# Performance work log

Measured on AMD Instinct MI355X. Metric: run time of the kernel, lower is better.

## Reference

```python
import jax, jax.numpy as jnp
import numpy as np

DEPTH = 100
HIDDEN = 1024
SHIFT = 25  # number of zeros prepended by the Shift module
LINEARITY = 0.97


def setup_inputs() -> dict:
    key = jax.random.key(0)
    ks = jax.random.split(key, 9)
    IN, OUT, B = 512, 512, 4096
    x = jax.random.normal(ks[0], (B, IN), dtype=jnp.float32)
    # torch Linear weight shape: [out, in]; xavier/kaiming init approximated by scaled normals
    fc1_w = jax.random.normal(ks[1], (HIDDEN, IN), dtype=jnp.float32) * (1.0 / np.sqrt(IN))
    fc1_b = jnp.zeros((HIDDEN,), dtype=jnp.float32)
    W1 = jax.random.normal(ks[2], (DEPTH, HIDDEN, HIDDEN), dtype=jnp.float32) * (1.0 / np.sqrt(HIDDEN))
    b1 = jnp.zeros((DEPTH, HIDDEN), dtype=jnp.float32)
    W2 = jax.random.normal(ks[3], (DEPTH, HIDDEN, HIDDEN), dtype=jnp.float32) * (np.sqrt(2.0) / np.sqrt(HIDDEN))
    b2 = jnp.zeros((DEPTH, HIDDEN), dtype=jnp.float32)
    fc2_w = jax.random.normal(ks[4], (OUT, HIDDEN), dtype=jnp.float32) * (1.0 / np.sqrt(HIDDEN))
    fc2_b = jnp.zeros((OUT,), dtype=jnp.float32)
    return {"x": x, "fc1_w": fc1_w, "fc1_b": fc1_b, "W1": W1, "b1": b1,
            "W2": W2, "b2": b2, "fc2_w": fc2_w, "fc2_b": fc2_b}


def _shift(x):
    # Shift: cat 25 zeros in front along last dim, then slice back to original width
    z = jnp.zeros_like(x[..., :SHIFT])
    return jnp.concatenate([z, x[..., :-SHIFT]], axis=-1)


def reference(x, fc1_w, fc1_b, W1, b1, W2, b2, fc2_w, fc2_b):
    x = x @ fc1_w.T + fc1_b  # [B, HIDDEN]

    def block(h, params):
        w1, bb1, w2, bb2 = params
        r = _shift(h)                       # shifted input is the residual
        a = jnp.maximum(r @ w1.T + bb1, 0)  # fc1 + clamp(min=0)
        y = a @ w2.T + bb2                  # fc2
        out = LINEARITY * r + (1.0 - LINEARITY) * y
        return out, None

    x, _ = jax.lax.scan(block, x, (W1, b1, W2, b2))
    return x @ fc2_w.T + fc2_b
```

## Files before the change

### kernel.cpp

```cpp
#include <hip/hip_runtime.h>
#include <cstdint>
#include <cstddef>

#define DEPTH 100
#define HID 1024
#define MROWS 4096

typedef _Float16 half8 __attribute__((ext_vector_type(8)));
typedef float floatx4 __attribute__((ext_vector_type(4)));

__device__ __forceinline__ void gload_lds16(const void* g, void* l) {
    __builtin_amdgcn_global_load_lds((const __attribute__((address_space(1))) void*)g,
                                     (__attribute__((address_space(3))) void*)l,
                                     16, 0, 0);
}

template<int MODE>
__global__ __launch_bounds__(512, 1)
void gemm_f(const _Float16* __restrict__ A, const _Float16* __restrict__ B,
            const float* __restrict__ bias, const float* __restrict__ hold,
            float* __restrict__ hnew, _Float16* __restrict__ rnext,
            _Float16* __restrict__ aout, float* __restrict__ outp,
            int N, int K, int rshift, int nbnl)
{
    __shared__ _Float16 As[3][128 * 64];
    __shared__ _Float16 Bs[3][128 * 64];

    const int tid = threadIdx.x;
    const int l   = tid & 63;
    const int w   = tid >> 6;
    const int wm  = w >> 2;
    const int wn  = w & 3;

    const int cpx = gridDim.x >> 3;
    const int b0  = blockIdx.x;
    const int bid = (b0 & 7) * cpx + (b0 >> 3);
    const int bn  = bid & ((1 << nbnl) - 1);
    const int bm  = bid >> nbnl;

    floatx4 acc[4][2];
    const floatx4 zero = {0.f, 0.f, 0.f, 0.f};
    #pragma unroll
    for (int i = 0; i < 4; ++i)
        #pragma unroll
        for (int j = 0; j < 2; ++j) acc[i][j] = zero;

    const int lr = l >> 3;
    const int lj = l & 7;
    const int sw = (l & 7) << 4;

    auto stage = [&](int buf, int kt) {
        #pragma unroll
        for (int q = 0; q < 2; ++q) {
            const int c   = w * 2 + q;
            const int row = c * 8 + lr;
            const int jch = lj ^ (row & 7);
            gload_lds16((const void*)(A + (size_t)(bm * 128 + row) * K + kt * 64 + jch * 8),
                        (void*)((char*)As[buf] + c * 1024));
        }
        #pragma unroll
        for (int q = 0; q < 2; ++q) {
            const int c   = w * 2 + q;
            const int row = c * 8 + lr;
            const int jch = lj ^ (row & 7);
            gload_lds16((const void*)(B + (size_t)(bn * 128 + row) * K + kt * 64 + jch * 8),
                        (void*)((char*)Bs[buf] + c * 1024));
        }
    };

    auto compute = [&](int buf) {
        #pragma unroll
        for (int kk = 0; kk < 2; ++kk) {
            half8 af[4], bf[2];
            #pragma unroll
            for (int fi = 0; fi < 4; ++fi) {
                const int off = ((wm * 64 + fi * 16 + (l & 15)) * 128 + kk * 64 + ((l >> 4) << 4)) ^ sw;
                af[fi] = *(const half8*)((const char*)As[buf] + off);
            }
            #pragma unroll
            for (int fj = 0; fj < 2; ++fj) {
                const int off = ((wn * 32 + fj * 16 + (l & 15)) * 128 + kk * 64 + ((l >> 4) << 4)) ^ sw;
                bf[fj] = *(const half8*)((const char*)Bs[buf] + off);
            }
            __builtin_amdgcn_s_setprio(1);
            #pragma unroll
            for (int fi = 0; fi < 4; ++fi)
                #pragma unroll
                for (int fj = 0; fj < 2; ++fj)
                    acc[fi][fj] = __builtin_amdgcn_mfma_f32_16x16x32_f16(af[fi], bf[fj], acc[fi][fj], 0, 0, 0);
            __builtin_amdgcn_s_setprio(0);
        }
    };

    const int nkt = K >> 6;
    stage(0, 0);
    if (nkt > 1) stage(1, 1);
    int cur = 0;
    for (int kt = 0; kt < nkt; ++kt) {
        if (kt + 2 < nkt) {
            int n2 = cur + 2; if (n2 >= 3) n2 -= 3;
            stage(n2, kt + 2);
        }
        const int rem   = nkt - 1 - kt;
        const int ahead = rem < 2 ? rem : 2;
        if (ahead == 2)      asm volatile("s_waitcnt vmcnt(8)" ::: "memory");
        else if (ahead == 1) asm volatile("s_waitcnt vmcnt(4)" ::: "memory");
        else                 asm volatile("s_waitcnt vmcnt(0)" ::: "memory");
        __builtin_amdgcn_s_barrier();
        __builtin_amdgcn_sched_barrier(0);
        compute(cur);
        __builtin_amdgcn_s_barrier();
        cur = (cur + 1 == 3) ? 0 : cur + 1;
    }

    const float C1 = 0.97f;
    const float C2 = (float)(1.0 - 0.97);
    const int colb = bn * 128 + wn * 32 + (l & 15);
    const int rowb = bm * 128 + wm * 64 + ((l >> 4) << 2);
    #pragma unroll
    for (int fi = 0; fi < 4; ++fi) {
        #pragma unroll
        for (int fj = 0; fj < 2; ++fj) {
            const int j = colb + fj * 16;
            const float bj = bias[j];
            #pragma unroll
            for (int v = 0; v < 4; ++v) {
                const int i = rowb + fi * 16 + v;
                const float val = acc[fi][fj][v] + bj;
                if constexpr (MODE == 1) {
                    aout[(size_t)i * N + j] = (_Float16)fmaxf(val, 0.f);
                } else if constexpr (MODE == 3) {
                    outp[(size_t)i * N + j] = val;
                } else {
                    float hv;
                    if constexpr (MODE == 2) {
                        const float rres = (j >= 25) ? hold[(size_t)i * N + j - 25] : 0.f;
                        hv = C1 * rres + C2 * val;
                    } else {
                        hv = val;
                    }
                    hnew[(size_t)i * N + j] = hv;
                    if (rshift == 0) {
                        rnext[(size_t)i * N + j] = (_Float16)hv;
                    } else {
                        if (j + 25 < N) rnext[(size_t)i * N + j + 25] = (_Float16)hv;
                        if (j < 25)     rnext[(size_t)i * N + j]      = (_Float16)0.f;
                    }
                }
            }
        }
    }
}

__global__ void cvt_kernel(const float* __restrict__ in, _Float16* __restrict__ out, long n8)
{
    const long stride = (long)gridDim.x * 256;
    for (long idx = (long)blockIdx.x * 256 + threadIdx.x; idx < n8; idx += stride) {
        const floatx4 f0 = ((const floatx4*)in)[idx * 2];
        const floatx4 f1 = ((const floatx4*)in)[idx * 2 + 1];
        half8 h;
        #pragma unroll
        for (int i = 0; i < 4; ++i) {
            h[i]     = (_Float16)f0[i];
            h[4 + i] = (_Float16)f1[i];
        }
        ((half8*)out)[idx] = h;
    }
}

static inline void launch_cvt(const float* in, _Float16* out, long n, hipStream_t s)
{
    const long n8 = n / 8;
    int blocks = (int)((n8 + 255) / 256);
    if (blocks > 2048) blocks = 2048;
    cvt_kernel<<<dim3(blocks), dim3(256), 0, s>>>(in, out, n8);
}

extern "C" void kernel_launch(void* const* d_in, const int* in_sizes, int n_in,
                              void* d_out, int out_size, void* d_ws, size_t ws_size,
                              hipStream_t stream)
{
    (void)in_sizes; (void)n_in; (void)out_size; (void)ws_size;
    const float* x     = (const float*)d_in[0];
    const float* fc1_w = (const float*)d_in[1];
    const float* fc1_b = (const float*)d_in[2];
    const float* W1    = (const float*)d_in[3];
    const float* b1    = (const float*)d_in[4];
    const float* W2    = (const float*)d_in[5];
    const float* b2    = (const float*)d_in[6];
    const float* fc2_w = (const float*)d_in[7];
    const float* fc2_b = (const float*)d_in[8];
    float* out = (float*)d_out;

    char* ws = (char*)d_ws;
    _Float16* xh = (_Float16*)(ws);
    _Float16* rb = (_Float16*)(ws + (4ull  << 20));
    _Float16* ab = (_Float16*)(ws + (12ull << 20));
    float*    h0 = (float*)   (ws + (20ull << 20));
    float*    h1 = (float*)   (ws + (36ull << 20));
    _Float16* fc1h = (_Float16*)(ws + (52ull  << 20));
    _Float16* fc2h = (_Float16*)(ws + (53ull  << 20));
    _Float16* W1h  = (_Float16*)(ws + (54ull  << 20));
    _Float16* W2h  = (_Float16*)(ws + (254ull << 20));

    launch_cvt(x, xh, (long)MROWS * 512, stream);
    launch_cvt(fc1_w, fc1h, (long)HID * 512, stream);
    launch_cvt(W1,    W1h,  (long)DEPTH * HID * HID, stream);
    launch_cvt(W2,    W2h,  (long)DEPTH * HID * HID, stream);
    launch_cvt(fc2_w, fc2h, (long)512 * HID, stream);

    gemm_f<0><<<dim3(32 * 8), dim3(512), 0, stream>>>(
        xh, fc1h, fc1_b, nullptr, h0, rb, nullptr, nullptr, HID, 512, 25, 3);

    for (int d = 0; d < DEPTH; ++d) {
        const _Float16* w1 = W1h + (size_t)d * HID * HID;
        const _Float16* w2 = W2h + (size_t)d * HID * HID;
        float* hold = (d & 1) ? h1 : h0;
        float* hnw  = (d & 1) ? h0 : h1;
        gemm_f<1><<<dim3(32 * 8), dim3(512), 0, stream>>>(
            rb, w1, b1 + (size_t)d * HID, nullptr, nullptr, nullptr, ab, nullptr,
            HID, HID, 0, 3);
        gemm_f<2><<<dim3(32 * 8), dim3(512), 0, stream>>>(
            ab, w2, b2 + (size_t)d * HID, hold, hnw, rb, nullptr, nullptr,
            HID, HID, (d == DEPTH - 1) ? 0 : 25, 3);
    }

    gemm_f<3><<<dim3(32 * 4), dim3(512), 0, stream>>>(
        rb, fc2h, fc2_b, nullptr, nullptr, nullptr, nullptr, out, 512, HID, 0, 2);
}
```

Baseline: 5.688 ms.

## Replace per-layer GEMM launches with one persistent kernel using grid barriers

Merges the 202 separate GEMM launches (fc1, 100 blocks of two GEMMs, fc2) into one persistent kernel of 256 workgroups. Dependent steps are separated by a global atomic-counter barrier in workspace, which is zeroed by a small kernel beforehand. The aim is to remove kernel launch overhead and the tail gaps between dependent launches. In exchange every step pays a spin-wait grid barrier. The kernel depends on all 256 workgroups being co-resident, and mode is now a runtime value rather than a template parameter, so it may use more registers.

After: 11.30 ms. +98.7%, slower.

```diff
diff --git a/kernel.cpp b/kernel.cpp
--- a/kernel.cpp
+++ b/kernel.cpp
@@ -5,6 +5,7 @@
 #define DEPTH 100
 #define HID 1024
 #define MROWS 4096
+#define NSTEPS 202
 
 typedef _Float16 half8 __attribute__((ext_vector_type(8)));
 typedef float floatx4 __attribute__((ext_vector_type(4)));
@@ -15,13 +16,15 @@
                                      16, 0, 0);
 }
 
-template<int MODE>
 __global__ __launch_bounds__(512, 1)
-void gemm_f(const _Float16* __restrict__ A, const _Float16* __restrict__ B,
-            const float* __restrict__ bias, const float* __restrict__ hold,
-            float* __restrict__ hnew, _Float16* __restrict__ rnext,
-            _Float16* __restrict__ aout, float* __restrict__ outp,
-            int N, int K, int rshift, int nbnl)
+void resnet_persist(const _Float16* __restrict__ xh, const _Float16* __restrict__ fc1h,
+                    const float* __restrict__ fc1_b,
+                    const _Float16* __restrict__ W1h, const float* __restrict__ b1,
+                    const _Float16* __restrict__ W2h, const float* __restrict__ b2,
+                    const _Float16* __restrict__ fc2h, const float* __restrict__ fc2_b,
+                    float* __restrict__ h0, float* __restrict__ h1,
+                    _Float16* __restrict__ rb, _Float16* __restrict__ ab,
+                    float* __restrict__ outp, unsigned* __restrict__ ctr)
 {
     __shared__ _Float16 As[3][128 * 64];
     __shared__ _Float16 Bs[3][128 * 64];
@@ -32,123 +35,168 @@
     const int wm  = w >> 2;
     const int wn  = w & 3;
 
-    const int cpx = gridDim.x >> 3;
     const int b0  = blockIdx.x;
-    const int bid = (b0 & 7) * cpx + (b0 >> 3);
-    const int bn  = bid & ((1 << nbnl) - 1);
-    const int bm  = bid >> nbnl;
-
-    floatx4 acc[4][2];
-    const floatx4 zero = {0.f, 0.f, 0.f, 0.f};
-    #pragma unroll
-    for (int i = 0; i < 4; ++i)
-        #pragma unroll
-        for (int j = 0; j < 2; ++j) acc[i][j] = zero;
+    const int bid = (b0 & 7) * 32 + (b0 >> 3);
 
     const int lr = l >> 3;
     const int lj = l & 7;
     const int sw = (l & 7) << 4;
 
-    auto stage = [&](int buf, int kt) {
-        #pragma unroll
-        for (int q = 0; q < 2; ++q) {
-            const int c   = w * 2 + q;
-            const int row = c * 8 + lr;
-            const int jch = lj ^ (row & 7);
-            gload_lds16((const void*)(A + (size_t)(bm * 128 + row) * K + kt * 64 + jch * 8),
-                        (void*)((char*)As[buf] + c * 1024));
-        }
-        #pragma unroll
-        for (int q = 0; q < 2; ++q) {
-            const int c   = w * 2 + q;
-            const int row = c * 8 + lr;
-            const int jch = lj ^ (row & 7);
-            gload_lds16((const void*)(B + (size_t)(bn * 128 + row) * K + kt * 64 + jch * 8),
-                        (void*)((char*)Bs[buf] + c * 1024));
-        }
-    };
-
-    auto compute = [&](int buf) {
-        #pragma unroll
-        for (int kk = 0; kk < 2; ++kk) {
-            half8 af[4], bf[2];
-            #pragma unroll
-            for (int fi = 0; fi < 4; ++fi) {
-                const int off = ((wm * 64 + fi * 16 + (l & 15)) * 128 + kk * 64 + ((l >> 4) << 4)) ^ sw;
-                af[fi] = *(const half8*)((const char*)As[buf] + off);
-            }
-            #pragma unroll
-            for (int fj = 0; fj < 2; ++fj) {
-                const int off = ((wn * 32 + fj * 16 + (l & 15)) * 128 + kk * 64 + ((l >> 4) << 4)) ^ sw;
-                bf[fj] = *(const half8*)((const char*)Bs[buf] + off);
-            }
-            __builtin_amdgcn_s_setprio(1);
-            #pragma unroll
-            for (int fi = 0; fi < 4; ++fi)
-                #pragma unroll
-                for (int fj = 0; fj < 2; ++fj)
-                    acc[fi][fj] = __builtin_amdgcn_mfma_f32_16x16x32_f16(af[fi], bf[fj], acc[fi][fj], 0, 0, 0);
-            __builtin_amdgcn_s_setprio(0);
-        }
-    };
-
-    const int nkt = K >> 6;
-    stage(0, 0);
-    if (nkt > 1) stage(1, 1);
-    int cur = 0;
-    for (int kt = 0; kt < nkt; ++kt) {
-        if (kt + 2 < nkt) {
-            int n2 = cur + 2; if (n2 >= 3) n2 -= 3;
-            stage(n2, kt + 2);
-        }
-        const int rem   = nkt - 1 - kt;
-        const int ahead = rem < 2 ? rem : 2;
-        if (ahead == 2)      asm volatile("s_waitcnt vmcnt(8)" ::: "memory");
-        else if (ahead == 1) asm volatile("s_waitcnt vmcnt(4)" ::: "memory");
-        else                 asm volatile("s_waitcnt vmcnt(0)" ::: "memory");
-        __builtin_amdgcn_s_barrier();
-        __builtin_amdgcn_sched_barrier(0);
-        compute(cur);
-        __builtin_amdgcn_s_barrier();
-        cur = (cur + 1 == 3) ? 0 : cur + 1;
-    }
-
     const float C1 = 0.97f;
     const float C2 = (float)(1.0 - 0.97);
-    const int colb = bn * 128 + wn * 32 + (l & 15);
-    const int rowb = bm * 128 + wm * 64 + ((l >> 4) << 2);
-    #pragma unroll
-    for (int fi = 0; fi < 4; ++fi) {
+
+    for (int s = 0; s < NSTEPS; ++s) {
+        if (s > 0) {
+            asm volatile("s_waitcnt vmcnt(0) lgkmcnt(0)" ::: "memory");
+            __syncthreads();
+            if (tid == 0) {
+                __hip_atomic_fetch_add(&ctr[s - 1], 1u, __ATOMIC_RELEASE, __HIP_MEMORY_SCOPE_AGENT);
+                while (__hip_atomic_load(&ctr[s - 1], __ATOMIC_RELAXED, __HIP_MEMORY_SCOPE_AGENT) < 256u) {
+                    __builtin_amdgcn_s_sleep(4);
+                }
+            }
+            __syncthreads();
+            __builtin_amdgcn_fence(__ATOMIC_ACQUIRE, "agent");
+        }
+
+        const _Float16* A; const _Float16* B; const float* bias;
+        const float* hold = nullptr; float* hnew = nullptr;
+        _Float16* rnext = nullptr; _Float16* aout = nullptr;
+        int K, mode, rshift = 0, Nout = HID;
+        if (s == 0) {
+            A = xh; B = fc1h; bias = fc1_b; K = 512; mode = 0;
+            hnew = h0; rnext = rb; rshift = 25;
+        } else if (s == NSTEPS - 1) {
+            A = rb; B = fc2h; bias = fc2_b; K = HID; mode = 3; Nout = 512;
+        } else {
+            const int d = (s - 1) >> 1;
+            if (s & 1) {
+                A = rb; B = W1h + (size_t)d * HID * HID; bias = b1 + d * HID;
+                K = HID; mode = 1; aout = ab;
+            } else {
+                A = ab; B = W2h + (size_t)d * HID * HID; bias = b2 + d * HID;
+                K = HID; mode = 2;
+                hold = (d & 1) ? h1 : h0; hnew = (d & 1) ? h0 : h1;
+                rnext = rb; rshift = (d == DEPTH - 1) ? 0 : 25;
+            }
+        }
+
+        int bm, bn; bool active = true;
+        if (mode == 3) {
+            if (bid < 128) { bm = bid >> 2; bn = bid & 3; }
+            else { active = false; bm = 0; bn = 0; }
+        } else {
+            bn = bid & 7; bm = bid >> 3;
+        }
+        if (!active) continue;
+
+        floatx4 acc[4][2];
+        const floatx4 zero = {0.f, 0.f, 0.f, 0.f};
         #pragma unroll
-        for (int fj = 0; fj < 2; ++fj) {
-            const int j = colb + fj * 16;
-            const float bj = bias[j];
-            #pragma unroll
-            for (int v = 0; v < 4; ++v) {
-                const int i = rowb + fi * 16 + v;
-                const float val = acc[fi][fj][v] + bj;
-                if constexpr (MODE == 1) {
-                    aout[(size_t)i * N + j] = (_Float16)fmaxf(val, 0.f);
-                } else if constexpr (MODE == 3) {
-                    outp[(size_t)i * N + j] = val;
-                } else {
-                    float hv;
-                    if constexpr (MODE == 2) {
-                        const float rres = (j >= 25) ? hold[(size_t)i * N + j - 25] : 0.f;
-                        hv = C1 * rres + C2 * val;
+        for (int i = 0; i < 4; ++i)
+            #pragma unroll
+            for (int j = 0; j < 2; ++j) acc[i][j] = zero;
+
+        auto stage = [&](int buf, int kt) {
+            #pragma unroll
+            for (int q = 0; q < 2; ++q) {
+                const int c   = w * 2 + q;
+                const int row = c * 8 + lr;
+                const int jch = lj ^ (row & 7);
+                gload_lds16((const void*)(A + (size_t)(bm * 128 + row) * K + kt * 64 + jch * 8),
+                            (void*)((char*)As[buf] + c * 1024));
+            }
+            #pragma unroll
+            for (int q = 0; q < 2; ++q) {
+                const int c   = w * 2 + q;
+                const int row = c * 8 + lr;
+                const int jch = lj ^ (row & 7);
+                gload_lds16((const void*)(B + (size_t)(bn * 128 + row) * K + kt * 64 + jch * 8),
+                            (void*)((char*)Bs[buf] + c * 1024));
+            }
+        };
+
+        auto compute = [&](int buf) {
+            #pragma unroll
+            for (int kk = 0; kk < 2; ++kk) {
+                half8 af[4], bf[2];
+                #pragma unroll
+                for (int fi = 0; fi < 4; ++fi) {
+                    const int off = ((wm * 64 + fi * 16 + (l & 15)) * 128 + kk * 64 + ((l >> 4) << 4)) ^ sw;
+                    af[fi] = *(const half8*)((const char*)As[buf] + off);
+                }
+                #pragma unroll
+                for (int fj = 0; fj < 2; ++fj) {
+                    const int off = ((wn * 32 + fj * 16 + (l & 15)) * 128 + kk * 64 + ((l >> 4) << 4)) ^ sw;
+                    bf[fj] = *(const half8*)((const char*)Bs[buf] + off);
+                }
+                __builtin_amdgcn_s_setprio(1);
+                #pragma unroll
+                for (int fi = 0; fi < 4; ++fi)
+                    #pragma unroll
+                    for (int fj = 0; fj < 2; ++fj)
+                        acc[fi][fj] = __builtin_amdgcn_mfma_f32_16x16x32_f16(af[fi], bf[fj], acc[fi][fj], 0, 0, 0);
+                __builtin_amdgcn_s_setprio(0);
+            }
+        };
+
+        const int nkt = K >> 6;
+        stage(0, 0);
+        stage(1, 1);
+        int cur = 0;
+        for (int kt = 0; kt < nkt; ++kt) {
+            if (kt + 2 < nkt) {
+                int n2 = cur + 2; if (n2 >= 3) n2 -= 3;
+                stage(n2, kt + 2);
+            }
+            const int rem   = nkt - 1 - kt;
+            const int ahead = rem < 2 ? rem : 2;
+            if (ahead == 2)      asm volatile("s_waitcnt vmcnt(8)" ::: "memory");
+            else if (ahead == 1) asm volatile("s_waitcnt vmcnt(4)" ::: "memory");
+            else                 asm volatile("s_waitcnt vmcnt(0)" ::: "memory");
+            __builtin_amdgcn_s_barrier();
+            __builtin_amdgcn_sched_barrier(0);
+            compute(cur);
+            __builtin_amdgcn_s_barrier();
+            cur = (cur + 1 == 3) ? 0 : cur + 1;
+        }
+
+        const int colb = bn * 128 + wn * 32 + (l & 15);
+        const int rowb = bm * 128 + wm * 64 + ((l >> 4) << 2);
+        #pragma unroll
+        for (int fi = 0; fi < 4; ++fi) {
+            #pragma unroll
+            for (int fj = 0; fj < 2; ++fj) {
+                const int j = colb + fj * 16;
+                const float bj = bias[j];
+                #pragma unroll
+                for (int v = 0; v < 4; ++v) {
+                    const int i = rowb + fi * 16 + v;
+                    const float val = acc[fi][fj][v] + bj;
+                    if (mode == 1) {
+                        aout[(size_t)i * HID + j] = (_Float16)fmaxf(val, 0.f);
+                    } else if (mode == 3) {
+                        outp[(size_t)i * 512 + j] = val;
                     } else {
-                        hv = val;
+                        float hv;
+                        if (mode == 2) {
+                            const float rres = (j >= 25) ? hold[(size_t)i * HID + j - 25] : 0.f;
+                            hv = C1 * rres + C2 * val;
+                        } else {
+                            hv = val;
+                        }
+                        hnew[(size_t)i * HID + j] = hv;
+                        if (rshift == 0) {
+                            rnext[(size_t)i * HID + j] = (_Float16)hv;
+                        } else {
+                            if (j + 25 < HID) rnext[(size_t)i * HID + j + 25] = (_Float16)hv;
+                            if (j < 25)       rnext[(size_t)i * HID + j]      = (_Float16)0.f;
+                        }
                     }
-                    hnew[(size_t)i * N + j] = hv;
-                    if (rshift == 0) {
-                        rnext[(size_t)i * N + j] = (_Float16)hv;
-                    } else {
-                        if (j + 25 < N) rnext[(size_t)i * N + j + 25] = (_Float16)hv;
-                        if (j < 25)     rnext[(size_t)i * N + j]      = (_Float16)0.f;
-                    }
-                }
-            }
-        }
+                }
+            }
+        }
+        (void)Nout;
     }
 }
 
@@ -166,6 +214,12 @@
         }
         ((half8*)out)[idx] = h;
     }
+}
+
+__global__ void zero_ctr(unsigned* __restrict__ ctr, int n)
+{
+    const int i = blockIdx.x * 256 + threadIdx.x;
+    if (i < n) ctr[i] = 0u;
 }
 
 static inline void launch_cvt(const float* in, _Float16* out, long n, hipStream_t s)
@@ -193,38 +247,25 @@
     float* out = (float*)d_out;
 
     char* ws = (char*)d_ws;
-    _Float16* xh = (_Float16*)(ws);
-    _Float16* rb = (_Float16*)(ws + (4ull  << 20));
-    _Float16* ab = (_Float16*)(ws + (12ull << 20));
-    float*    h0 = (float*)   (ws + (20ull << 20));
-    float*    h1 = (float*)   (ws + (36ull << 20));
+    _Float16* xh   = (_Float16*)(ws);
+    _Float16* rb   = (_Float16*)(ws + (4ull   << 20));
+    _Float16* ab   = (_Float16*)(ws + (12ull  << 20));
+    float*    h0   = (float*)   (ws + (20ull  << 20));
+    float*    h1   = (float*)   (ws + (36ull  << 20));
     _Float16* fc1h = (_Float16*)(ws + (52ull  << 20));
     _Float16* fc2h = (_Float16*)(ws + (53ull  << 20));
     _Float16* W1h  = (_Float16*)(ws + (54ull  << 20));
     _Float16* W2h  = (_Float16*)(ws + (254ull << 20));
+    unsigned* ctr  = (unsigned*)(ws + (460ull << 20));
 
     launch_cvt(x, xh, (long)MROWS * 512, stream);
     launch_cvt(fc1_w, fc1h, (long)HID * 512, stream);
     launch_cvt(W1,    W1h,  (long)DEPTH * HID * HID, stream);
     launch_cvt(W2,    W2h,  (long)DEPTH * HID * HID, stream);
     launch_cvt(fc2_w, fc2h, (long)512 * HID, stream);
-
-    gemm_f<0><<<dim3(32 * 8), dim3(512), 0, stream>>>(
-        xh, fc1h, fc1_b, nullptr, h0, rb, nullptr, nullptr, HID, 512, 25, 3);
-
-    for (int d = 0; d < DEPTH; ++d) {
-        const _Float16* w1 = W1h + (size_t)d * HID * HID;
-        const _Float16* w2 = W2h + (size_t)d * HID * HID;
-        float* hold = (d & 1) ? h1 : h0;
-        float* hnw  = (d & 1) ? h0 : h1;
-        gemm_f<1><<<dim3(32 * 8), dim3(512), 0, stream>>>(
-            rb, w1, b1 + (size_t)d * HID, nullptr, nullptr, nullptr, ab, nullptr,
-            HID, HID, 0, 3);
-        gemm_f<2><<<dim3(32 * 8), dim3(512), 0, stream>>>(
-            ab, w2, b2 + (size_t)d * HID, hold, hnw, rb, nullptr, nullptr,
-            HID, HID, (d == DEPTH - 1) ? 0 : 25, 3);
-    }
-
-    gemm_f<3><<<dim3(32 * 4), dim3(512), 0, stream>>>(
-        rb, fc2h, fc2_b, nullptr, nullptr, nullptr, nullptr, out, 512, HID, 0, 2);
-}
+    zero_ctr<<<dim3(1), dim3(256), 0, stream>>>(ctr, NSTEPS + 2);
+
+    resnet_persist<<<dim3(256), dim3(512), 0, stream>>>(
+        xh, fc1h, fc1_b, W1h, b1, W2h, b2, fc2h, fc2_b,
+        h0, h1, rb, ab, out, ctr);
+}
```
